# Performance work log

Measured on AMD Instinct MI355X. Metric: run time of the kernel, lower is better.

## Reference

```python
import jax, jax.numpy as jnp
import numpy as np

N_NODES = 100000


def setup_inputs() -> dict:
    key = jax.random.key(0)
    k1, k2, k3, k4, k5, k6 = jax.random.split(key, 6)
    n_edges = 1600000
    X = jax.random.normal(k1, (N_NODES, 256), dtype=jnp.float32)
    edge_row = jax.random.randint(k2, (n_edges,), 0, N_NODES, dtype=jnp.int64)
    edge_col = jax.random.randint(k3, (n_edges,), 0, N_NODES, dtype=jnp.int64)
    edge_val = jax.random.uniform(k4, (n_edges,), dtype=jnp.float32)
    W = jax.random.normal(k5, (128, 256), dtype=jnp.float32) * 0.05
    b = jax.random.normal(k6, (128,), dtype=jnp.float32) * 0.05
    return {"X": X, "edge_row": edge_row, "edge_col": edge_col,
            "edge_val": edge_val, "W": W, "b": b}


def reference(X, edge_row, edge_col, edge_val, W, b):
    # Dense projection: H = X @ W^T + b  -> [N, out_dim]
    H = jnp.einsum('ni,oi->no', X, W) + b
    # SpMM: out[r] = sum_e A[r, c_e] * H[c_e] over edges with row r
    msgs = edge_val[:, None] * H[edge_col]          # [E, out_dim]
    out = jax.ops.segment_sum(msgs, edge_row, num_segments=N_NODES)
    return out
```

## Files before the change

kernel.cpp:

```cpp
#include <hip/hip_runtime.h>
#include <hip/hip_bf16.h>

#define NNODES 100000
#define NEDGES 1600000
#define KDIM 256
#define ODIM 128
#define NXCD 8
#define NB_SCAN 391
#define EDGE_CAP 1900032
#define GEMM_BLOCKS 1563
#define EDGE_BLOCKS 1563
#define CONV_BLOCKS 128
#define ZERO_BLOCKS 3125

typedef __attribute__((ext_vector_type(8))) short short8;
typedef __attribute__((ext_vector_type(4))) float floatx4;

static __device__ __forceinline__ short f2bf(float f) {
  union { float f; unsigned u; } x; x.f = f;
  unsigned r = (x.u + 0x7fffu + ((x.u >> 16) & 1u)) >> 16;
  return (short)r;
}

__global__ __launch_bounds__(256) void init_kernel(
    const float* __restrict__ W, short* __restrict__ Wb,
    unsigned* __restrict__ counts) {
  if (blockIdx.x < CONV_BLOCKS) {
    int i = blockIdx.x * 256 + threadIdx.x;
    if (i < ODIM * KDIM) Wb[i] = f2bf(W[i]);
    return;
  }
  int i = (blockIdx.x - CONV_BLOCKS) * 256 + threadIdx.x;
  if (i < NXCD * NNODES) counts[i] = 0u;
}

__global__ __launch_bounds__(256) void gemm_rank_kernel(
    const float* __restrict__ X, const short* __restrict__ Wb,
    const float* __restrict__ bias, unsigned* __restrict__ H2,
    const int* __restrict__ rows, unsigned* __restrict__ counts,
    unsigned short* __restrict__ rank) {
  if (blockIdx.x >= GEMM_BLOCKS) {
    unsigned xcc;
    asm("s_getreg_b32 %0, hwreg(HW_REG_XCC_ID)" : "=s"(xcc));
    xcc &= 7u;
    unsigned* cbase = counts + (size_t)xcc * NNODES;
    const int e0 = ((blockIdx.x - GEMM_BLOCKS) * 256 + threadIdx.x) * 4;
    if (e0 < NEDGES) {
      const int4 r4 = *(const int4*)(rows + e0);
      const unsigned o0 = __hip_atomic_fetch_add(&cbase[r4.x], 1u, __ATOMIC_RELAXED,
                                                 __HIP_MEMORY_SCOPE_WORKGROUP);
      const unsigned o1 = __hip_atomic_fetch_add(&cbase[r4.y], 1u, __ATOMIC_RELAXED,
                                                 __HIP_MEMORY_SCOPE_WORKGROUP);
      const unsigned o2 = __hip_atomic_fetch_add(&cbase[r4.z], 1u, __ATOMIC_RELAXED,
                                                 __HIP_MEMORY_SCOPE_WORKGROUP);
      const unsigned o3 = __hip_atomic_fetch_add(&cbase[r4.w], 1u, __ATOMIC_RELAXED,
                                                 __HIP_MEMORY_SCOPE_WORKGROUP);
      ushort4 rk;
      rk.x = (unsigned short)((xcc << 8) | o0);
      rk.y = (unsigned short)((xcc << 8) | o1);
      rk.z = (unsigned short)((xcc << 8) | o2);
      rk.w = (unsigned short)((xcc << 8) | o3);
      *(ushort4*)(rank + e0) = rk;
    }
    return;
  }
  const int lane = threadIdx.x & 63;
  const int wave = threadIdx.x >> 6;
  const int l16 = lane & 15;
  const int quad = lane >> 4;
  const int rowBase = blockIdx.x * 64 + wave * 16;
  const int arow = rowBase + l16;
  const bool inb = arow < NNODES;
  const float4 zf4 = {0.f, 0.f, 0.f, 0.f};
  const float4* xp = (const float4*)(X + (size_t)(inb ? arow : 0) * KDIM + quad * 8);

  floatx4 acc[8];
#pragma unroll
  for (int t = 0; t < 8; t++) acc[t] = (floatx4){0.f, 0.f, 0.f, 0.f};

  float4 c0 = inb ? xp[0] : zf4;
  float4 c1 = inb ? xp[1] : zf4;
#pragma unroll
  for (int k0 = 0; k0 < 8; k0++) {
    float4 n0, n1;
    if (k0 < 7) {
      n0 = inb ? xp[(k0 + 1) * 8] : zf4;
      n1 = inb ? xp[(k0 + 1) * 8 + 1] : zf4;
    }
    short8 a;
    a[0] = f2bf(c0.x); a[1] = f2bf(c0.y); a[2] = f2bf(c0.z); a[3] = f2bf(c0.w);
    a[4] = f2bf(c1.x); a[5] = f2bf(c1.y); a[6] = f2bf(c1.z); a[7] = f2bf(c1.w);
    const short* bp = Wb + k0 * 32 + quad * 8;
#pragma unroll
    for (int t = 0; t < 8; t++) {
      short8 b = *(const short8*)(bp + (size_t)(t * 16 + l16) * KDIM);
      acc[t] = __builtin_amdgcn_mfma_f32_16x16x32_bf16(a, b, acc[t], 0, 0, 0);
    }
    if (k0 < 7) { c0 = n0; c1 = n1; }
  }

#pragma unroll
  for (int t = 0; t < 4; t++) {
    const int cl = t * 16 + l16;
    const float blo = bias[cl];
    const float bhi = bias[cl + 64];
#pragma unroll
    for (int r = 0; r < 4; r++) {
      const int row = rowBase + quad * 4 + r;
      if (row < NNODES) {
        unsigned lo = (unsigned short)f2bf(acc[t][r] + blo);
        unsigned hi = (unsigned short)f2bf(acc[t + 4][r] + bhi);
        H2[(size_t)row * 64 + cl] = lo | (hi << 16);
      }
    }
  }
}

__global__ __launch_bounds__(256) void scan1_kernel(
    const unsigned* __restrict__ counts, int* __restrict__ chunkExcl,
    int* __restrict__ blockSums) {
  __shared__ int s[256];
  int t = threadIdx.x;
  int n = blockIdx.x * 256 + t;
  int sum = 0;
  if (n < NNODES) {
    int s0 = 0;
#pragma unroll
    for (int x = 0; x < NXCD; x++) s0 += (int)counts[(size_t)x * NNODES + n];
    sum = (s0 + 3) & ~3;
  }
  s[t] = sum;
  __syncthreads();
  for (int o = 1; o < 256; o <<= 1) {
    int add = (t >= o) ? s[t - o] : 0;
    __syncthreads();
    s[t] += add;
    __syncthreads();
  }
  if (n < NNODES) chunkExcl[n] = s[t] - sum;
  if (t == 255) blockSums[blockIdx.x] = s[255];
}

__global__ __launch_bounds__(512) void scan23_kernel(
    const int* __restrict__ blockSums, const int* __restrict__ chunkExcl,
    unsigned* __restrict__ counts, int* __restrict__ offsets,
    int2* __restrict__ edges) {
  __shared__ int s[512];
  const int t = threadIdx.x;
  s[t] = (t < NB_SCAN) ? blockSums[t] : 0;
  __syncthreads();
  for (int o = 1; o < 512; o <<= 1) {
    int add = (t >= o) ? s[t - o] : 0;
    __syncthreads();
    s[t] += add;
    __syncthreads();
  }
  const int myBase = (blockIdx.x == 0) ? 0 : s[blockIdx.x - 1];
  if (blockIdx.x == 0 && t == 0) offsets[NNODES] = s[NB_SCAN - 1];
  if (t < 256) {
    const int n = blockIdx.x * 256 + t;
    if (n < NNODES) {
      const int run = chunkExcl[n] + myBase;
      offsets[n] = run;
      int c[NXCD];
      int deg = 0;
#pragma unroll
      for (int x = 0; x < NXCD; x++) {
        c[x] = (int)counts[(size_t)x * NNODES + n];
        deg += c[x];
      }
      int acc2 = run;
#pragma unroll
      for (int x = 0; x < NXCD; x++) {
        counts[(size_t)x * NNODES + n] = (unsigned)acc2;
        acc2 += c[x];
      }
      const int padded = (deg + 3) & ~3;
      const int2 zrec = {0, 0};
      for (int p = run + deg; p < run + padded; p++) edges[p] = zrec;
    }
  }
}

__global__ __launch_bounds__(256) void place_kernel(
    const int* __restrict__ rows, const int* __restrict__ cols,
    const float* __restrict__ vals, const unsigned short* __restrict__ rank,
    const unsigned* __restrict__ sbase, int2* __restrict__ edges) {
  const int e0 = (blockIdx.x * 256 + threadIdx.x) * 4;
  if (e0 < NEDGES) {
    const int4 r4 = *(const int4*)(rows + e0);
    const int4 c4 = *(const int4*)(cols + e0);
    const float4 v4 = *(const float4*)(vals + e0);
    const ushort4 k4 = *(const ushort4*)(rank + e0);
    int2 rec;
    rec.x = c4.x; rec.y = __float_as_int(v4.x);
    edges[(int)sbase[(size_t)(k4.x >> 8) * NNODES + r4.x] + (int)(k4.x & 255u)] = rec;
    rec.x = c4.y; rec.y = __float_as_int(v4.y);
    edges[(int)sbase[(size_t)(k4.y >> 8) * NNODES + r4.y] + (int)(k4.y & 255u)] = rec;
    rec.x = c4.z; rec.y = __float_as_int(v4.z);
    edges[(int)sbase[(size_t)(k4.z >> 8) * NNODES + r4.z] + (int)(k4.z & 255u)] = rec;
    rec.x = c4.w; rec.y = __float_as_int(v4.w);
    edges[(int)sbase[(size_t)(k4.w >> 8) * NNODES + r4.w] + (int)(k4.w & 255u)] = rec;
  }
}

__global__ __launch_bounds__(256) void spmm_kernel(const int* __restrict__ offsets,
                                                   const int2* __restrict__ edges,
                                                   const unsigned* __restrict__ H2,
                                                   float* __restrict__ out) {
  const int lane = threadIdx.x & 63;
  const int row = blockIdx.x * 4 + (threadIdx.x >> 6);
  if (row >= NNODES) return;
  const int s = offsets[row];
  const int e = offsets[row + 1];
  float ax = 0.f, ay = 0.f;
  for (int i = s; i < e; i += 4) {
    const int4 p01 = *(const int4*)(edges + i);
    const int4 p23 = *(const int4*)(edges + i + 2);
    const unsigned h0 = H2[(size_t)p01.x * 64 + lane];
    const unsigned h1 = H2[(size_t)p01.z * 64 + lane];
    const unsigned h2 = H2[(size_t)p23.x * 64 + lane];
    const unsigned h3 = H2[(size_t)p23.z * 64 + lane];
    const float v0 = __int_as_float(p01.y);
    const float v1 = __int_as_float(p01.w);
    const float v2 = __int_as_float(p23.y);
    const float v3 = __int_as_float(p23.w);
    ax += v0 * __uint_as_float(h0 << 16);
    ay += v0 * __uint_as_float(h0 & 0xffff0000u);
    ax += v1 * __uint_as_float(h1 << 16);
    ay += v1 * __uint_as_float(h1 & 0xffff0000u);
    ax += v2 * __uint_as_float(h2 << 16);
    ay += v2 * __uint_as_float(h2 & 0xffff0000u);
    ax += v3 * __uint_as_float(h3 << 16);
    ay += v3 * __uint_as_float(h3 & 0xffff0000u);
  }
  out[(size_t)row * 128 + lane] = ax;
  out[(size_t)row * 128 + 64 + lane] = ay;
}

extern "C" void kernel_launch(void* const* d_in, const int* in_sizes, int n_in,
                              void* d_out, int out_size, void* d_ws, size_t ws_size,
                              hipStream_t stream) {
  const float* X = (const float*)d_in[0];
  const int* erow = (const int*)d_in[1];
  const int* ecol = (const int*)d_in[2];
  const float* eval = (const float*)d_in[3];
  const float* W = (const float*)d_in[4];
  const float* bias = (const float*)d_in[5];
  float* out = (float*)d_out;

  char* ws = (char*)d_ws;
  size_t off = 0;
  auto alloc = [&](size_t bytes) -> char* {
    char* p = ws + off;
    off += (bytes + 255) & ~(size_t)255;
    return p;
  };
  unsigned* Hb = (unsigned*)alloc((size_t)NNODES * 64 * 4);
  short* Wb = (short*)alloc((size_t)ODIM * KDIM * 2);
  unsigned* counts = (unsigned*)alloc((size_t)NXCD * NNODES * 4);
  int* chunkExcl = (int*)alloc((size_t)NNODES * 4);
  int* offsets = (int*)alloc((size_t)(NNODES + 1) * 4);
  int* blockSums = (int*)alloc((size_t)NB_SCAN * 4);
  unsigned short* rank = (unsigned short*)alloc((size_t)NEDGES * 2);
  int2* edges = (int2*)alloc((size_t)EDGE_CAP * 8);

  init_kernel<<<CONV_BLOCKS + ZERO_BLOCKS, 256, 0, stream>>>(W, Wb, counts);
  gemm_rank_kernel<<<GEMM_BLOCKS + EDGE_BLOCKS, 256, 0, stream>>>(X, Wb, bias, Hb,
                                                                  erow, counts, rank);
  scan1_kernel<<<NB_SCAN, 256, 0, stream>>>(counts, chunkExcl, blockSums);
  scan23_kernel<<<NB_SCAN, 512, 0, stream>>>(blockSums, chunkExcl, counts, offsets, edges);
  place_kernel<<<EDGE_BLOCKS, 256, 0, stream>>>(erow, ecol, eval, rank, counts, edges);
  spmm_kernel<<<(NNODES + 3) / 4, 256, 0, stream>>>(offsets, edges, (const unsigned*)Hb, out);
}
```

Baseline: 378.8 us.

## Stage GEMM X tiles via global_load_lds with swizzle; unroll SpMM gather by 8

The GEMM path now copies each block's 64x256 fp32 X tile into LDS in two halves using direct global-to-LDS loads with an XOR swizzle, then reads A fragments from LDS instead of doing strided per-lane global loads. The SpMM loop is unrolled to eight edges per iteration with a four-edge tail, which puts more independent H2 gathers in flight. The GEMM change adds 32KB of LDS per block (also allocated by the counting blocks) and barriers, which may reduce occupancy. The SpMM tail relies on rows being padded to multiples of four.

```diff
diff --git a/kernel.cpp b/kernel.cpp
--- a/kernel.cpp
+++ b/kernel.cpp
@@ -39,6 +39,7 @@
     const float* __restrict__ bias, unsigned* __restrict__ H2,
     const int* __restrict__ rows, unsigned* __restrict__ counts,
     unsigned short* __restrict__ rank) {
+  __shared__ float As[64 * 128];
   if (blockIdx.x >= GEMM_BLOCKS) {
     unsigned xcc;
     asm("s_getreg_b32 %0, hwreg(HW_REG_XCC_ID)" : "=s"(xcc));
@@ -68,35 +69,48 @@
   const int wave = threadIdx.x >> 6;
   const int l16 = lane & 15;
   const int quad = lane >> 4;
-  const int rowBase = blockIdx.x * 64 + wave * 16;
-  const int arow = rowBase + l16;
-  const bool inb = arow < NNODES;
-  const float4 zf4 = {0.f, 0.f, 0.f, 0.f};
-  const float4* xp = (const float4*)(X + (size_t)(inb ? arow : 0) * KDIM + quad * 8);
+  const int bRow0 = blockIdx.x * 64;
+  const int rowBase = bRow0 + wave * 16;
+  const int rl = wave * 16 + l16;
+  const int sw = (l16 & 7) * 4;
 
   floatx4 acc[8];
 #pragma unroll
   for (int t = 0; t < 8; t++) acc[t] = (floatx4){0.f, 0.f, 0.f, 0.f};
 
-  float4 c0 = inb ? xp[0] : zf4;
-  float4 c1 = inb ? xp[1] : zf4;
-#pragma unroll
-  for (int k0 = 0; k0 < 8; k0++) {
-    float4 n0, n1;
-    if (k0 < 7) {
-      n0 = inb ? xp[(k0 + 1) * 8] : zf4;
-      n1 = inb ? xp[(k0 + 1) * 8 + 1] : zf4;
-    }
-    short8 a;
-    a[0] = f2bf(c0.x); a[1] = f2bf(c0.y); a[2] = f2bf(c0.z); a[3] = f2bf(c0.w);
-    a[4] = f2bf(c1.x); a[5] = f2bf(c1.y); a[6] = f2bf(c1.z); a[7] = f2bf(c1.w);
-    const short* bp = Wb + k0 * 32 + quad * 8;
-#pragma unroll
-    for (int t = 0; t < 8; t++) {
-      short8 b = *(const short8*)(bp + (size_t)(t * 16 + l16) * KDIM);
-      acc[t] = __builtin_amdgcn_mfma_f32_16x16x32_bf16(a, b, acc[t], 0, 0, 0);
-    }
-    if (k0 < 7) { c0 = n0; c1 = n1; }
+#pragma unroll
+  for (int h = 0; h < 2; h++) {
+#pragma unroll
+    for (int j = 0; j < 8; j++) {
+      const int r0 = wave * 16 + j * 2;
+      const int rlane = r0 + (lane >> 5);
+      int grow = bRow0 + rlane;
+      if (grow >= NNODES) grow = NNODES - 1;
+      const int csrc = (((lane & 31) * 4) ^ ((rlane & 7) * 4));
+      const float* src = X + (size_t)grow * KDIM + h * 128 + csrc;
+      __builtin_amdgcn_global_load_lds(
+          (const __attribute__((address_space(1))) void*)src,
+          (__attribute__((address_space(3))) void*)(&As[r0 * 128]),
+          16, 0, 0);
+    }
+    __syncthreads();
+#pragma unroll
+    for (int k0i = 0; k0i < 4; k0i++) {
+      const int k0 = h * 4 + k0i;
+      const int c = k0i * 32 + quad * 8;
+      const float4 c0 = *(const float4*)&As[rl * 128 + (c ^ sw)];
+      const float4 c1 = *(const float4*)&As[rl * 128 + ((c + 4) ^ sw)];
+      short8 a;
+      a[0] = f2bf(c0.x); a[1] = f2bf(c0.y); a[2] = f2bf(c0.z); a[3] = f2bf(c0.w);
+      a[4] = f2bf(c1.x); a[5] = f2bf(c1.y); a[6] = f2bf(c1.z); a[7] = f2bf(c1.w);
+      const short* bp = Wb + k0 * 32 + quad * 8;
+#pragma unroll
+      for (int t = 0; t < 8; t++) {
+        short8 b = *(const short8*)(bp + (size_t)(t * 16 + l16) * KDIM);
+        acc[t] = __builtin_amdgcn_mfma_f32_16x16x32_bf16(a, b, acc[t], 0, 0, 0);
+      }
+    }
+    if (h == 0) __syncthreads();
   }
 
 #pragma unroll
@@ -214,17 +228,50 @@
   const int s = offsets[row];
   const int e = offsets[row + 1];
   float ax = 0.f, ay = 0.f;
-  for (int i = s; i < e; i += 4) {
+  int i = s;
+  for (; i + 8 <= e; i += 8) {
+    const int4 p01 = *(const int4*)(edges + i);
+    const int4 p23 = *(const int4*)(edges + i + 2);
+    const int4 p45 = *(const int4*)(edges + i + 4);
+    const int4 p67 = *(const int4*)(edges + i + 6);
+    const unsigned h0 = H2[(size_t)p01.x * 64 + lane];
+    const unsigned h1 = H2[(size_t)p01.z * 64 + lane];
+    const unsigned h2 = H2[(size_t)p23.x * 64 + lane];
+    const unsigned h3 = H2[(size_t)p23.z * 64 + lane];
+    const unsigned h4 = H2[(size_t)p45.x * 64 + lane];
+    const unsigned h5 = H2[(size_t)p45.z * 64 + lane];
+    const unsigned h6 = H2[(size_t)p67.x * 64 + lane];
+    const unsigned h7 = H2[(size_t)p67.z * 64 + lane];
+    const float v0 = __int_as_float(p01.y), v1 = __int_as_float(p01.w);
+    const float v2 = __int_as_float(p23.y), v3 = __int_as_float(p23.w);
+    const float v4 = __int_as_float(p45.y), v5 = __int_as_float(p45.w);
+    const float v6 = __int_as_float(p67.y), v7 = __int_as_float(p67.w);
+    ax += v0 * __uint_as_float(h0 << 16);
+    ay += v0 * __uint_as_float(h0 & 0xffff0000u);
+    ax += v1 * __uint_as_float(h1 << 16);
+    ay += v1 * __uint_as_float(h1 & 0xffff0000u);
+    ax += v2 * __uint_as_float(h2 << 16);
+    ay += v2 * __uint_as_float(h2 & 0xffff0000u);
+    ax += v3 * __uint_as_float(h3 << 16);
+    ay += v3 * __uint_as_float(h3 & 0xffff0000u);
+    ax += v4 * __uint_as_float(h4 << 16);
+    ay += v4 * __uint_as_float(h4 & 0xffff0000u);
+    ax += v5 * __uint_as_float(h5 << 16);
+    ay += v5 * __uint_as_float(h5 & 0xffff0000u);
+    ax += v6 * __uint_as_float(h6 << 16);
+    ay += v6 * __uint_as_float(h6 & 0xffff0000u);
+    ax += v7 * __uint_as_float(h7 << 16);
+    ay += v7 * __uint_as_float(h7 & 0xffff0000u);
+  }
+  if (i < e) {
     const int4 p01 = *(const int4*)(edges + i);
     const int4 p23 = *(const int4*)(edges + i + 2);
     const unsigned h0 = H2[(size_t)p01.x * 64 + lane];
     const unsigned h1 = H2[(size_t)p01.z * 64 + lane];
     const unsigned h2 = H2[(size_t)p23.x * 64 + lane];
     const unsigned h3 = H2[(size_t)p23.z * 64 + lane];
-    const float v0 = __int_as_float(p01.y);
-    const float v1 = __int_as_float(p01.w);
-    const float v2 = __int_as_float(p23.y);
-    const float v3 = __int_as_float(p23.w);
+    const float v0 = __int_as_float(p01.y), v1 = __int_as_float(p01.w);
+    const float v2 = __int_as_float(p23.y), v3 = __int_as_float(p23.w);
     ax += v0 * __uint_as_float(h0 << 16);
     ay += v0 * __uint_as_float(h0 & 0xffff0000u);
     ax += v1 * __uint_as_float(h1 << 16);
```

Result: faster. 371.2 us (-2.0%).
